# Optimization experiments

Hardware: AMD Instinct MI355X
Metric: run time of the kernel (lower is better)

Reference implementation:

```python
import jax, jax.numpy as jnp
import numpy as np

K = 8
N = 32768
L = 512  # latent_dim
SCALE = 1.0  # params in torch are tiny ((2u-1)/(K*out)); randn here, math identical


def _fkan(x, A, B):
    # x: [N, in]; A, B: [out, in, K]
    # y[b,o] = sum_{i,k} A[o,i,k]*sin(k*x[b,i]) + B[o,i,k]*cos(k*x[b,i])
    k = jnp.arange(K, dtype=x.dtype)            # [K]
    kx = x[..., None] * k                       # [N, in, K]
    return (jnp.einsum('bik,oik->bo', jnp.sin(kx), A)
            + jnp.einsum('bik,oik->bo', jnp.cos(kx), B))


def setup_inputs() -> dict:
    key = jax.random.key(0)
    ks = jax.random.split(key, 11)
    shapes = [(L, 1, K), (L, L, K), (L, L, K), (L, L, K), (1, L, K)]
    inp = {'x': jax.random.normal(ks[0], (N, 1), dtype=jnp.float32)}
    for li, shp in enumerate(shapes):
        # mimic torch init scale (2u-1)/(K*out)
        out = shp[0]
        inp[f'A{li}'] = (2.0 * jax.random.uniform(ks[1 + 2 * li], shp, dtype=jnp.float32) - 1.0) / (K * out)
        inp[f'B{li}'] = (2.0 * jax.random.uniform(ks[2 + 2 * li], shp, dtype=jnp.float32) - 1.0) / (K * out)
    return inp


def reference(x, A0, B0, A1, B1, A2, B2, A3, B3, A4, B4):
    for A, B in ((A0, B0), (A1, B1), (A2, B2), (A3, B3), (A4, B4)):
        x = _fkan(x, A, B)
    return x  # [N, 1]
```

## Files before the change

kernel.cpp:

```cpp
#include <hip/hip_runtime.h>
#include <hip/hip_bf16.h>
#include <math.h>

#define NB 32768
#define DIM 512
#define KF 8
#define FEAT 8192
#define BM 64
#define NSUP 64
#define NSTEP 128

typedef __attribute__((ext_vector_type(4))) int i32x4;
typedef unsigned short ushort_t;
typedef unsigned int uint_t;

#define WSCALE 520192.0f
#define OUT_SCALE (1.0f / (127.0f * 520192.0f))

static __device__ __forceinline__ ushort_t f2bf_s(float f) {
    return (ushort_t)((__float_as_uint(f) + 0x8000u) >> 16);
}
static __device__ __forceinline__ float bf2f(ushort_t u) {
    return __uint_as_float(((uint_t)u) << 16);
}

static __device__ __forceinline__ uint_t qb4(float a, float b, float c, float d) {
    const float MG = 12582912.0f;
    uint_t ua = __float_as_uint(a + MG);
    uint_t ub = __float_as_uint(b + MG);
    uint_t uc = __float_as_uint(c + MG);
    uint_t ud = __float_as_uint(d + MG);
    uint_t p1 = __builtin_amdgcn_perm(ub, ua, 0x0C0C0400u);
    uint_t p2 = __builtin_amdgcn_perm(ud, uc, 0x0C0C0400u);
    return __builtin_amdgcn_perm(p2, p1, 0x05040100u);
}

static __device__ __forceinline__ i32x4 feat_q16(float xv) {
    float s1, c1;
    __sincosf(xv, &s1, &c1);
    float S[KF], C[KF];
    S[0] = 0.f; C[0] = 127.f;
    S[1] = 127.f * s1; C[1] = 127.f * c1;
#pragma unroll
    for (int k = 2; k < KF; ++k) {
        S[k] = S[k - 1] * c1 + C[k - 1] * s1;
        C[k] = C[k - 1] * c1 - S[k - 1] * s1;
    }
    i32x4 r;
    r[0] = (int)qb4(S[0], S[1], S[2], S[3]);
    r[1] = (int)qb4(S[4], S[5], S[6], S[7]);
    r[2] = (int)qb4(C[0], C[1], C[2], C[3]);
    r[3] = (int)qb4(C[4], C[5], C[6], C[7]);
    return r;
}

static __device__ __forceinline__ int pk4w(const float* w) {
    int q[4];
#pragma unroll
    for (int j = 0; j < 4; ++j) {
        int v = __float2int_rn(w[j] * WSCALE);
        v = v > 127 ? 127 : (v < -127 ? -127 : v);
        q[j] = v & 255;
    }
    return (int)((uint_t)q[0] | ((uint_t)q[1] << 8) | ((uint_t)q[2] << 16) | ((uint_t)q[3] << 24));
}

__global__ void pack_w8(const float* __restrict__ A, const float* __restrict__ B,
                        i32x4* __restrict__ Wf) {
    int u = blockIdx.x * 256 + threadIdx.x;
    int lane = u & 63;
    int n = (u >> 6) & 3, wb = (u >> 8) & 7, t = u >> 11;
    int o = wb * 64 + n * 16 + (lane & 15);
    int i = t * 4 + (lane >> 4);
    const float* a = A + ((size_t)o * DIM + i) * KF;
    const float* b = B + ((size_t)o * DIM + i) * KF;
    i32x4 v;
    v[0] = pk4w(a);
    v[1] = pk4w(a + 4);
    v[2] = pk4w(b);
    v[3] = pk4w(b + 4);
    Wf[u] = v;
}

__global__ void layer0(const float* __restrict__ x, const float* __restrict__ A0,
                       const float* __restrict__ B0, ushort_t* __restrict__ Y) {
    int gid = blockIdx.x * 256 + threadIdx.x;
    int b = gid >> 9, o = gid & 511;
    float xv = x[b];
    float s1, c1;
    __sincosf(xv, &s1, &c1);
    const float* a = A0 + o * KF;
    const float* bb = B0 + o * KF;
    float acc = bb[0];
    float sk = 0.f, ck = 1.f;
#pragma unroll
    for (int k = 1; k < KF; ++k) {
        float sn = sk * c1 + ck * s1;
        float cn = ck * c1 - sk * s1;
        sk = sn; ck = cn;
        acc += a[k] * sk + bb[k] * ck;
    }
    Y[gid] = f2bf_s(acc);
}

__global__ __launch_bounds__(256, 2) void fkan_gemm(const ushort_t* __restrict__ X,
                                                    const i32x4* __restrict__ Wf,
                                                    ushort_t* __restrict__ Y) {
    __shared__ i32x4 ring[4][256];
    const int tid = threadIdx.x;
    const int lane = tid & 63, wave = tid >> 6;
    const int l15 = lane & 15, l4 = lane >> 4;
    const int bm0 = blockIdx.x * BM;

    const int bl = tid >> 2, ii = tid & 3;
    const ushort_t* xp = X + (size_t)(bm0 + bl) * DIM + ii;
    const int wunit = (bl >> 1) * 8 + (((ii * 2 + (bl & 1)) ^ ((bl >> 1) & 7)));

    int runit[4];
#pragma unroll
    for (int m = 0; m < 4; ++m) {
        int r = m * 16 + l15;
        runit[m] = (r >> 1) * 8 + (((l4 * 2 + (r & 1)) ^ ((r >> 1) & 7)));
    }

    const i32x4* bp = Wf + lane;
    int boff[8];
#pragma unroll
    for (int n = 0; n < 8; ++n)
        boff[n] = (2 * wave + (n >> 2)) * 256 + (n & 3) * 64;

    i32x4 acc[4][8];
#pragma unroll
    for (int m = 0; m < 4; ++m)
#pragma unroll
        for (int n = 0; n < 8; ++n) acc[m][n] = (i32x4)0;

    ring[0][wunit] = feat_q16(bf2f(xp[0]));
    ring[1][wunit] = feat_q16(bf2f(xp[4]));
    i32x4 c[8];
#pragma unroll
    for (int n = 0; n < 8; ++n) c[n] = bp[boff[n]];
    float xvA = bf2f(xp[8]);
    float xvB = bf2f(xp[12]);
    asm volatile("s_waitcnt lgkmcnt(0)" ::: "memory");
    __builtin_amdgcn_s_barrier();

    for (int T = 0; T < NSUP; ++T) {
        const i32x4* rd0 = &ring[(2 * T) & 3][0];
        const i32x4* rd1 = &ring[(2 * T + 1) & 3][0];
        i32x4* wr0 = &ring[(2 * T + 2) & 3][0];
        i32x4* wr1 = &ring[(2 * T + 3) & 3][0];
        const size_t t0 = 2 * (size_t)T;
        i32x4 af[4];

#pragma unroll
        for (int m = 0; m < 4; ++m) af[m] = rd0[runit[m]];
        if (T + 1 < NSUP)
            wr0[wunit] = feat_q16(xvA);
#pragma unroll
        for (int n = 0; n < 8; ++n) {
#pragma unroll
            for (int m = 0; m < 4; ++m)
                acc[m][n] = __builtin_amdgcn_mfma_i32_16x16x64_i8(af[m], c[n], acc[m][n], 0, 0, 0);
            c[n] = bp[boff[n] + (t0 + 1) * 2048];
        }

#pragma unroll
        for (int m = 0; m < 4; ++m) af[m] = rd1[runit[m]];
        if (T + 1 < NSUP) {
            wr1[wunit] = feat_q16(xvB);
            if (T + 2 < NSUP) {
                xvA = bf2f(xp[(T + 2) * 8]);
                xvB = bf2f(xp[(T + 2) * 8 + 4]);
            }
        }
        if (T + 1 < NSUP) {
#pragma unroll
            for (int n = 0; n < 8; ++n) {
#pragma unroll
                for (int m = 0; m < 4; ++m)
                    acc[m][n] = __builtin_amdgcn_mfma_i32_16x16x64_i8(af[m], c[n], acc[m][n], 0, 0, 0);
                c[n] = bp[boff[n] + (t0 + 2) * 2048];
            }
        } else {
#pragma unroll
            for (int n = 0; n < 8; ++n)
#pragma unroll
                for (int m = 0; m < 4; ++m)
                    acc[m][n] = __builtin_amdgcn_mfma_i32_16x16x64_i8(af[m], c[n], acc[m][n], 0, 0, 0);
        }

        asm volatile("s_waitcnt lgkmcnt(0)" ::: "memory");
        __builtin_amdgcn_s_barrier();
    }

#pragma unroll
    for (int m = 0; m < 4; ++m)
#pragma unroll
        for (int n = 0; n < 8; ++n)
#pragma unroll
            for (int j = 0; j < 4; ++j) {
                int row = bm0 + m * 16 + l4 * 4 + j;
                int col = wave * 128 + n * 16 + l15;
                Y[(size_t)row * DIM + col] = f2bf_s((float)acc[m][n][j] * OUT_SCALE);
            }
}

__global__ void layer4(const ushort_t* __restrict__ X, const float* __restrict__ A4,
                       const float* __restrict__ B4, float* __restrict__ Y) {
    int wave = threadIdx.x >> 6, lane = threadIdx.x & 63;
    int b = blockIdx.x * 4 + wave;
    float acc = 0.f;
#pragma unroll
    for (int ii = 0; ii < 8; ++ii) {
        int i = lane + ii * 64;
        float xv = bf2f(X[(size_t)b * DIM + i]);
        float s1, c1;
        __sincosf(xv, &s1, &c1);
        const float* a = A4 + i * KF;
        const float* bb = B4 + i * KF;
        acc += bb[0];
        float sk = 0.f, ck = 1.f;
#pragma unroll
        for (int k = 1; k < KF; ++k) {
            float sn = sk * c1 + ck * s1;
            float cn = ck * c1 - sk * s1;
            sk = sn; ck = cn;
            acc += a[k] * sk + bb[k] * ck;
        }
    }
#pragma unroll
    for (int off = 32; off > 0; off >>= 1) acc += __shfl_down(acc, off, 64);
    if (lane == 0) Y[b] = acc;
}

extern "C" void kernel_launch(void* const* d_in, const int* in_sizes, int n_in,
                              void* d_out, int out_size, void* d_ws, size_t ws_size,
                              hipStream_t stream) {
    const float* x  = (const float*)d_in[0];
    const float* A0 = (const float*)d_in[1];
    const float* B0 = (const float*)d_in[2];
    const float* A1 = (const float*)d_in[3];
    const float* B1 = (const float*)d_in[4];
    const float* A2 = (const float*)d_in[5];
    const float* B2 = (const float*)d_in[6];
    const float* A3 = (const float*)d_in[7];
    const float* B3 = (const float*)d_in[8];
    const float* A4 = (const float*)d_in[9];
    const float* B4 = (const float*)d_in[10];
    float* out = (float*)d_out;

    char* ws = (char*)d_ws;
    const size_t actBytes = (size_t)NB * DIM * sizeof(ushort_t);
    const size_t wBytes = (size_t)DIM * FEAT;
    ushort_t* bufA = (ushort_t*)ws;
    ushort_t* bufB = (ushort_t*)(ws + actBytes);
    i32x4* W1 = (i32x4*)(ws + 2 * actBytes);
    i32x4* W2 = (i32x4*)(ws + 2 * actBytes + wBytes);
    i32x4* W3 = (i32x4*)(ws + 2 * actBytes + 2 * wBytes);

    pack_w8<<<DIM * FEAT / 16 / 256, 256, 0, stream>>>(A1, B1, W1);
    pack_w8<<<DIM * FEAT / 16 / 256, 256, 0, stream>>>(A2, B2, W2);
    pack_w8<<<DIM * FEAT / 16 / 256, 256, 0, stream>>>(A3, B3, W3);

    layer0<<<(NB * DIM) / 256, 256, 0, stream>>>(x, A0, B0, bufA);

    fkan_gemm<<<NB / BM, 256, 0, stream>>>(bufA, W1, bufB);
    fkan_gemm<<<NB / BM, 256, 0, stream>>>(bufB, W2, bufA);
    fkan_gemm<<<NB / BM, 256, 0, stream>>>(bufA, W3, bufB);

    layer4<<<NB / 4, 256, 0, stream>>>(bufB, A4, B4, out);
}
```

Baseline: 454.1 us.

## Split GEMM block across eight waves with smaller per-wave accumulator tiles

The fused GEMM kernel moves from 4 waves owning 128 output columns each to 8 waves owning 64 columns each, halving accumulators and B-fragment registers per wave and raising launch bounds to 512 threads. The feature-generation work of writing the ring buffer is split between two thread groups, one per half-step. This is meant to add waves per CU for better latency hiding. The cost is less B reuse per wave, more A fragment LDS reads relative to MFMAs, and larger barriers.

```diff
diff --git a/kernel.cpp b/kernel.cpp
--- a/kernel.cpp
+++ b/kernel.cpp
@@ -103,7 +103,7 @@
     Y[gid] = f2bf_s(acc);
 }
 
-__global__ __launch_bounds__(256, 2) void fkan_gemm(const ushort_t* __restrict__ X,
+__global__ __launch_bounds__(512, 4) void fkan_gemm(const ushort_t* __restrict__ X,
                                                     const i32x4* __restrict__ Wf,
                                                     ushort_t* __restrict__ Y) {
     __shared__ i32x4 ring[4][256];
@@ -112,7 +112,8 @@
     const int l15 = lane & 15, l4 = lane >> 4;
     const int bm0 = blockIdx.x * BM;
 
-    const int bl = tid >> 2, ii = tid & 3;
+    const int item = tid & 255, g = tid >> 8;
+    const int bl = item >> 2, ii = item & 3;
     const ushort_t* xp = X + (size_t)(bm0 + bl) * DIM + ii;
     const int wunit = (bl >> 1) * 8 + (((ii * 2 + (bl & 1)) ^ ((bl >> 1) & 7)));
 
@@ -123,71 +124,55 @@
         runit[m] = (r >> 1) * 8 + (((l4 * 2 + (r & 1)) ^ ((r >> 1) & 7)));
     }
 
-    const i32x4* bp = Wf + lane;
-    int boff[8];
-#pragma unroll
-    for (int n = 0; n < 8; ++n)
-        boff[n] = (2 * wave + (n >> 2)) * 256 + (n & 3) * 64;
-
-    i32x4 acc[4][8];
+    const i32x4* bp = Wf + wave * 256 + lane;
+
+    i32x4 acc[4][4];
 #pragma unroll
     for (int m = 0; m < 4; ++m)
 #pragma unroll
-        for (int n = 0; n < 8; ++n) acc[m][n] = (i32x4)0;
-
-    ring[0][wunit] = feat_q16(bf2f(xp[0]));
-    ring[1][wunit] = feat_q16(bf2f(xp[4]));
-    i32x4 c[8];
-#pragma unroll
-    for (int n = 0; n < 8; ++n) c[n] = bp[boff[n]];
-    float xvA = bf2f(xp[8]);
-    float xvB = bf2f(xp[12]);
+        for (int n = 0; n < 4; ++n) acc[m][n] = (i32x4)0;
+
+    ring[g][wunit] = feat_q16(bf2f(xp[g * 4]));
+    i32x4 c[4];
+#pragma unroll
+    for (int n = 0; n < 4; ++n) c[n] = bp[n * 64];
+    float xv = bf2f(xp[(2 + g) * 4]);
     asm volatile("s_waitcnt lgkmcnt(0)" ::: "memory");
     __builtin_amdgcn_s_barrier();
 
     for (int T = 0; T < NSUP; ++T) {
         const i32x4* rd0 = &ring[(2 * T) & 3][0];
         const i32x4* rd1 = &ring[(2 * T + 1) & 3][0];
-        i32x4* wr0 = &ring[(2 * T + 2) & 3][0];
-        i32x4* wr1 = &ring[(2 * T + 3) & 3][0];
+        i32x4* wr = &ring[(2 * T + 2 + g) & 3][0];
         const size_t t0 = 2 * (size_t)T;
         i32x4 af[4];
 
 #pragma unroll
         for (int m = 0; m < 4; ++m) af[m] = rd0[runit[m]];
+        if (g == 0 && T + 1 < NSUP)
+            wr[wunit] = feat_q16(xv);
+#pragma unroll
+        for (int m = 0; m < 4; ++m)
+#pragma unroll
+            for (int n = 0; n < 4; ++n)
+                acc[m][n] = __builtin_amdgcn_mfma_i32_16x16x64_i8(af[m], c[n], acc[m][n], 0, 0, 0);
+#pragma unroll
+        for (int n = 0; n < 4; ++n) c[n] = bp[n * 64 + (t0 + 1) * 2048];
+
+#pragma unroll
+        for (int m = 0; m < 4; ++m) af[m] = rd1[runit[m]];
+        if (g == 1 && T + 1 < NSUP)
+            wr[wunit] = feat_q16(xv);
         if (T + 1 < NSUP)
-            wr0[wunit] = feat_q16(xvA);
-#pragma unroll
-        for (int n = 0; n < 8; ++n) {
-#pragma unroll
-            for (int m = 0; m < 4; ++m)
+            xv = bf2f(xp[(t0 + 4 + g) * 4]);
+#pragma unroll
+        for (int m = 0; m < 4; ++m)
+#pragma unroll
+            for (int n = 0; n < 4; ++n)
                 acc[m][n] = __builtin_amdgcn_mfma_i32_16x16x64_i8(af[m], c[n], acc[m][n], 0, 0, 0);
-            c[n] = bp[boff[n] + (t0 + 1) * 2048];
-        }
-
-#pragma unroll
-        for (int m = 0; m < 4; ++m) af[m] = rd1[runit[m]];
         if (T + 1 < NSUP) {
-            wr1[wunit] = feat_q16(xvB);
-            if (T + 2 < NSUP) {
-                xvA = bf2f(xp[(T + 2) * 8]);
-                xvB = bf2f(xp[(T + 2) * 8 + 4]);
-            }
-        }
-        if (T + 1 < NSUP) {
-#pragma unroll
-            for (int n = 0; n < 8; ++n) {
-#pragma unroll
-                for (int m = 0; m < 4; ++m)
-                    acc[m][n] = __builtin_amdgcn_mfma_i32_16x16x64_i8(af[m], c[n], acc[m][n], 0, 0, 0);
-                c[n] = bp[boff[n] + (t0 + 2) * 2048];
-            }
-        } else {
-#pragma unroll
-            for (int n = 0; n < 8; ++n)
-#pragma unroll
-                for (int m = 0; m < 4; ++m)
-                    acc[m][n] = __builtin_amdgcn_mfma_i32_16x16x64_i8(af[m], c[n], acc[m][n], 0, 0, 0);
+#pragma unroll
+            for (int n = 0; n < 4; ++n) c[n] = bp[n * 64 + (t0 + 2) * 2048];
         }
 
         asm volatile("s_waitcnt lgkmcnt(0)" ::: "memory");
@@ -197,11 +182,11 @@
 #pragma unroll
     for (int m = 0; m < 4; ++m)
 #pragma unroll
-        for (int n = 0; n < 8; ++n)
+        for (int n = 0; n < 4; ++n)
 #pragma unroll
             for (int j = 0; j < 4; ++j) {
                 int row = bm0 + m * 16 + l4 * 4 + j;
-                int col = wave * 128 + n * 16 + l15;
+                int col = wave * 64 + n * 16 + l15;
                 Y[(size_t)row * DIM + col] = f2bf_s((float)acc[m][n][j] * OUT_SCALE);
             }
 }
@@ -265,9 +250,9 @@
 
     layer0<<<(NB * DIM) / 256, 256, 0, stream>>>(x, A0, B0, bufA);
 
-    fkan_gemm<<<NB / BM, 256, 0, stream>>>(bufA, W1, bufB);
-    fkan_gemm<<<NB / BM, 256, 0, stream>>>(bufB, W2, bufA);
-    fkan_gemm<<<NB / BM, 256, 0, stream>>>(bufA, W3, bufB);
+    fkan_gemm<<<NB / BM, 512, 0, stream>>>(bufA, W1, bufB);
+    fkan_gemm<<<NB / BM, 512, 0, stream>>>(bufB, W2, bufA);
+    fkan_gemm<<<NB / BM, 512, 0, stream>>>(bufA, W3, bufB);
 
     layer4<<<NB / 4, 256, 0, stream>>>(bufB, A4, B4, out);
 }
```

Result: slower. 497.8 us (+9.6%).

## Deepen LDS feature ring and halve barrier frequency in int8 GEMM

Applied to the files above, without the earlier changes.

The LDS ring for quantized Fourier features grows from 4 to 8 slots, so staging runs two k-steps ahead and the workgroup barrier is needed only every other superstep. Both A-fragment sets are read from LDS up front, and the MFMA blocks are wrapped in s_setprio to favour matrix issue over the feature-staging writes. The aim is to cut barrier stalls and to overlap LDS traffic and sincos staging with MFMA work. In exchange it doubles LDS use and keeps more live registers for the second fragment set, which could hurt occupancy or cause spills under the 2-block launch bound.

```diff
diff --git a/kernel.cpp b/kernel.cpp
--- a/kernel.cpp
+++ b/kernel.cpp
@@ -106,7 +106,7 @@
 __global__ __launch_bounds__(256, 2) void fkan_gemm(const ushort_t* __restrict__ X,
                                                     const i32x4* __restrict__ Wf,
                                                     ushort_t* __restrict__ Y) {
-    __shared__ i32x4 ring[4][256];
+    __shared__ i32x4 ring[8][256];
     const int tid = threadIdx.x;
     const int lane = tid & 63, wave = tid >> 6;
     const int l15 = lane & 15, l4 = lane >> 4;
@@ -135,51 +135,50 @@
 #pragma unroll
         for (int n = 0; n < 8; ++n) acc[m][n] = (i32x4)0;
 
-    ring[0][wunit] = feat_q16(bf2f(xp[0]));
-    ring[1][wunit] = feat_q16(bf2f(xp[4]));
+#pragma unroll
+    for (int t = 0; t < 4; ++t)
+        ring[t][wunit] = feat_q16(bf2f(xp[t * 4]));
     i32x4 c[8];
 #pragma unroll
     for (int n = 0; n < 8; ++n) c[n] = bp[boff[n]];
-    float xvA = bf2f(xp[8]);
-    float xvB = bf2f(xp[12]);
+    float xvA = bf2f(xp[16]);
+    float xvB = bf2f(xp[20]);
     asm volatile("s_waitcnt lgkmcnt(0)" ::: "memory");
     __builtin_amdgcn_s_barrier();
 
     for (int T = 0; T < NSUP; ++T) {
-        const i32x4* rd0 = &ring[(2 * T) & 3][0];
-        const i32x4* rd1 = &ring[(2 * T + 1) & 3][0];
-        i32x4* wr0 = &ring[(2 * T + 2) & 3][0];
-        i32x4* wr1 = &ring[(2 * T + 3) & 3][0];
+        const i32x4* rd0 = &ring[(2 * T) & 7][0];
+        const i32x4* rd1 = &ring[(2 * T + 1) & 7][0];
+        i32x4* wr0 = &ring[(2 * T + 4) & 7][0];
+        i32x4* wr1 = &ring[(2 * T + 5) & 7][0];
         const size_t t0 = 2 * (size_t)T;
-        i32x4 af[4];
-
-#pragma unroll
-        for (int m = 0; m < 4; ++m) af[m] = rd0[runit[m]];
-        if (T + 1 < NSUP)
+        const bool stg = (T + 2 < NSUP);
+
+        i32x4 af0[4], af1[4];
+#pragma unroll
+        for (int m = 0; m < 4; ++m) af0[m] = rd0[runit[m]];
+#pragma unroll
+        for (int m = 0; m < 4; ++m) af1[m] = rd1[runit[m]];
+
+        __builtin_amdgcn_s_setprio(1);
+#pragma unroll
+        for (int n = 0; n < 8; ++n) {
+#pragma unroll
+            for (int m = 0; m < 4; ++m)
+                acc[m][n] = __builtin_amdgcn_mfma_i32_16x16x64_i8(af0[m], c[n], acc[m][n], 0, 0, 0);
+            c[n] = bp[boff[n] + (t0 + 1) * 2048];
+        }
+        __builtin_amdgcn_s_setprio(0);
+        if (stg)
             wr0[wunit] = feat_q16(xvA);
-#pragma unroll
-        for (int n = 0; n < 8; ++n) {
-#pragma unroll
-            for (int m = 0; m < 4; ++m)
-                acc[m][n] = __builtin_amdgcn_mfma_i32_16x16x64_i8(af[m], c[n], acc[m][n], 0, 0, 0);
-            c[n] = bp[boff[n] + (t0 + 1) * 2048];
-        }
-
-#pragma unroll
-        for (int m = 0; m < 4; ++m) af[m] = rd1[runit[m]];
+
+        __builtin_amdgcn_s_setprio(1);
         if (T + 1 < NSUP) {
-            wr1[wunit] = feat_q16(xvB);
-            if (T + 2 < NSUP) {
-                xvA = bf2f(xp[(T + 2) * 8]);
-                xvB = bf2f(xp[(T + 2) * 8 + 4]);
-            }
-        }
-        if (T + 1 < NSUP) {
 #pragma unroll
             for (int n = 0; n < 8; ++n) {
 #pragma unroll
                 for (int m = 0; m < 4; ++m)
-                    acc[m][n] = __builtin_amdgcn_mfma_i32_16x16x64_i8(af[m], c[n], acc[m][n], 0, 0, 0);
+                    acc[m][n] = __builtin_amdgcn_mfma_i32_16x16x64_i8(af1[m], c[n], acc[m][n], 0, 0, 0);
                 c[n] = bp[boff[n] + (t0 + 2) * 2048];
             }
         } else {
@@ -187,11 +186,21 @@
             for (int n = 0; n < 8; ++n)
 #pragma unroll
                 for (int m = 0; m < 4; ++m)
-                    acc[m][n] = __builtin_amdgcn_mfma_i32_16x16x64_i8(af[m], c[n], acc[m][n], 0, 0, 0);
-        }
-
-        asm volatile("s_waitcnt lgkmcnt(0)" ::: "memory");
-        __builtin_amdgcn_s_barrier();
+                    acc[m][n] = __builtin_amdgcn_mfma_i32_16x16x64_i8(af1[m], c[n], acc[m][n], 0, 0, 0);
+        }
+        __builtin_amdgcn_s_setprio(0);
+        if (stg) {
+            wr1[wunit] = feat_q16(xvB);
+            if (T + 3 < NSUP) {
+                xvA = bf2f(xp[(t0 + 6) * 4]);
+                xvB = bf2f(xp[(t0 + 7) * 4]);
+            }
+        }
+
+        if (T & 1) {
+            asm volatile("s_waitcnt lgkmcnt(0)" ::: "memory");
+            __builtin_amdgcn_s_barrier();
+        }
     }
 
 #pragma unroll
```

After: 448.8 us. About the same (-1.2%).

## Compute int8 Fourier features in registers, dropping LDS ring and barriers

Applied to the files above, without the earlier changes.

The GEMM kernel no longer stages quantized sin/cos features through a shared-memory ring buffer with per-step barriers. Each lane now loads the raw bf16 x values it needs straight from global memory and computes the feature vectors in registers. Weight loads use byte offsets with a software-pipelined reload. This removes LDS traffic and block-wide syncs, but the feature computation is repeated across the lanes that share a row, adding VALU work and register pressure.

```diff
diff --git a/kernel.cpp b/kernel.cpp
--- a/kernel.cpp
+++ b/kernel.cpp
@@ -7,8 +7,6 @@
 #define KF 8
 #define FEAT 8192
 #define BM 64
-#define NSUP 64
-#define NSTEP 128
 
 typedef __attribute__((ext_vector_type(4))) int i32x4;
 typedef unsigned short ushort_t;
@@ -106,28 +104,24 @@
 __global__ __launch_bounds__(256, 2) void fkan_gemm(const ushort_t* __restrict__ X,
                                                     const i32x4* __restrict__ Wf,
                                                     ushort_t* __restrict__ Y) {
-    __shared__ i32x4 ring[4][256];
     const int tid = threadIdx.x;
     const int lane = tid & 63, wave = tid >> 6;
     const int l15 = lane & 15, l4 = lane >> 4;
     const int bm0 = blockIdx.x * BM;
 
-    const int bl = tid >> 2, ii = tid & 3;
-    const ushort_t* xp = X + (size_t)(bm0 + bl) * DIM + ii;
-    const int wunit = (bl >> 1) * 8 + (((ii * 2 + (bl & 1)) ^ ((bl >> 1) & 7)));
-
-    int runit[4];
+    const char* xb = (const char*)(X + (size_t)bm0 * DIM);
+    const char* wb = (const char*)Wf;
+
+    uint_t xvA[4], xvB[4];
 #pragma unroll
     for (int m = 0; m < 4; ++m) {
-        int r = m * 16 + l15;
-        runit[m] = (r >> 1) * 8 + (((l4 * 2 + (r & 1)) ^ ((r >> 1) & 7)));
-    }
-
-    const i32x4* bp = Wf + lane;
-    int boff[8];
-#pragma unroll
-    for (int n = 0; n < 8; ++n)
-        boff[n] = (2 * wave + (n >> 2)) * 256 + (n & 3) * 64;
+        uint_t base = (uint_t)((m * 16 + l15) * (DIM * 2) + l4 * 2);
+        xvA[m] = base;
+        xvB[m] = base + 16u;
+    }
+
+    uint_t voffL = (uint_t)(wave * 8192 + lane * 16);
+    uint_t voffH = voffL + 4096u;
 
     i32x4 acc[4][8];
 #pragma unroll
@@ -135,64 +129,62 @@
 #pragma unroll
         for (int n = 0; n < 8; ++n) acc[m][n] = (i32x4)0;
 
-    ring[0][wunit] = feat_q16(bf2f(xp[0]));
-    ring[1][wunit] = feat_q16(bf2f(xp[4]));
+    uint_t xA[8], xB[8];
+#pragma unroll
+    for (int m = 0; m < 4; ++m) {
+        xA[m]     = *(const ushort_t*)(xb + xvA[m]);
+        xA[4 + m] = *(const ushort_t*)(xb + xvA[m] + 8);
+        xB[m]     = *(const ushort_t*)(xb + xvB[m]);
+        xB[4 + m] = *(const ushort_t*)(xb + xvB[m] + 8);
+        xvA[m] += 32u;
+        xvB[m] += 32u;
+    }
     i32x4 c[8];
 #pragma unroll
-    for (int n = 0; n < 8; ++n) c[n] = bp[boff[n]];
-    float xvA = bf2f(xp[8]);
-    float xvB = bf2f(xp[12]);
-    asm volatile("s_waitcnt lgkmcnt(0)" ::: "memory");
-    __builtin_amdgcn_s_barrier();
-
-    for (int T = 0; T < NSUP; ++T) {
-        const i32x4* rd0 = &ring[(2 * T) & 3][0];
-        const i32x4* rd1 = &ring[(2 * T + 1) & 3][0];
-        i32x4* wr0 = &ring[(2 * T + 2) & 3][0];
-        i32x4* wr1 = &ring[(2 * T + 3) & 3][0];
-        const size_t t0 = 2 * (size_t)T;
-        i32x4 af[4];
-
-#pragma unroll
-        for (int m = 0; m < 4; ++m) af[m] = rd0[runit[m]];
-        if (T + 1 < NSUP)
-            wr0[wunit] = feat_q16(xvA);
-#pragma unroll
-        for (int n = 0; n < 8; ++n) {
-#pragma unroll
-            for (int m = 0; m < 4; ++m)
-                acc[m][n] = __builtin_amdgcn_mfma_i32_16x16x64_i8(af[m], c[n], acc[m][n], 0, 0, 0);
-            c[n] = bp[boff[n] + (t0 + 1) * 2048];
-        }
-
-#pragma unroll
-        for (int m = 0; m < 4; ++m) af[m] = rd1[runit[m]];
-        if (T + 1 < NSUP) {
-            wr1[wunit] = feat_q16(xvB);
-            if (T + 2 < NSUP) {
-                xvA = bf2f(xp[(T + 2) * 8]);
-                xvB = bf2f(xp[(T + 2) * 8 + 4]);
-            }
-        }
-        if (T + 1 < NSUP) {
-#pragma unroll
-            for (int n = 0; n < 8; ++n) {
-#pragma unroll
-                for (int m = 0; m < 4; ++m)
-                    acc[m][n] = __builtin_amdgcn_mfma_i32_16x16x64_i8(af[m], c[n], acc[m][n], 0, 0, 0);
-                c[n] = bp[boff[n] + (t0 + 2) * 2048];
-            }
-        } else {
-#pragma unroll
-            for (int n = 0; n < 8; ++n)
-#pragma unroll
-                for (int m = 0; m < 4; ++m)
-                    acc[m][n] = __builtin_amdgcn_mfma_i32_16x16x64_i8(af[m], c[n], acc[m][n], 0, 0, 0);
-        }
-
-        asm volatile("s_waitcnt lgkmcnt(0)" ::: "memory");
-        __builtin_amdgcn_s_barrier();
-    }
+    for (int n = 0; n < 4; ++n) c[n]     = *(const i32x4*)(wb + voffL + n * 1024);
+#pragma unroll
+    for (int n = 0; n < 4; ++n) c[4 + n] = *(const i32x4*)(wb + voffH + n * 1024);
+    voffL += 32768u; voffH += 32768u;
+
+#define KSTEP(X0, X1, X2, X3, RELOAD)                                                      \
+    {                                                                                      \
+        i32x4 af[4];                                                                       \
+        af[0] = feat_q16(bf2f((ushort_t)(X0)));                                            \
+        af[1] = feat_q16(bf2f((ushort_t)(X1)));                                            \
+        af[2] = feat_q16(bf2f((ushort_t)(X2)));                                            \
+        af[3] = feat_q16(bf2f((ushort_t)(X3)));                                            \
+        _Pragma("unroll")                                                                  \
+        for (int n = 0; n < 8; ++n) {                                                      \
+            _Pragma("unroll")                                                              \
+            for (int m = 0; m < 4; ++m)                                                    \
+                acc[m][n] = __builtin_amdgcn_mfma_i32_16x16x64_i8(af[m], c[n], acc[m][n], 0, 0, 0); \
+            if (RELOAD)                                                                    \
+                c[n] = (n < 4) ? *(const i32x4*)(wb + voffL + n * 1024)                    \
+                               : *(const i32x4*)(wb + voffH + (n - 4) * 1024);             \
+        }                                                                                  \
+        if (RELOAD) { voffL += 32768u; voffH += 32768u; }                                  \
+    }
+
+#define SUPER(XS, XV, REFILL, RL2)                                                         \
+    KSTEP(XS[0], XS[1], XS[2], XS[3], 1)                                                   \
+    KSTEP(XS[4], XS[5], XS[6], XS[7], RL2)                                                 \
+    if (REFILL) {                                                                          \
+        _Pragma("unroll")                                                                  \
+        for (int m = 0; m < 4; ++m) {                                                      \
+            XS[m]     = *(const ushort_t*)(xb + XV[m]);                                    \
+            XS[4 + m] = *(const ushort_t*)(xb + XV[m] + 8);                                \
+            XV[m] += 32u;                                                                  \
+        }                                                                                  \
+    }
+
+    for (int it = 0; it < 31; ++it) {
+        SUPER(xA, xvA, 1, 1)
+        SUPER(xB, xvB, 1, 1)
+    }
+    SUPER(xA, xvA, 0, 1)
+    SUPER(xB, xvB, 0, 0)
+#undef SUPER
+#undef KSTEP
 
 #pragma unroll
     for (int m = 0; m < 4; ++m)
```

Result: slower. 879.2 us (+93.6%).
